# Kernel tuning notes

Measured on AMD Instinct MI355X. Metric: run time of the kernel, lower is better.

The kernel has to match this reference:

```python
import jax, jax.numpy as jnp
import numpy as np
from jax import lax

WINDOW = 8
MAX_VAL = 1.0
C1 = (0.01 * MAX_VAL) ** 2
C2 = (0.03 * MAX_VAL) ** 2


def _box_sum(x):
    # Equivalent to conv2d with an all-ones WINDOW x WINDOW kernel, groups=C, VALID padding.
    return lax.reduce_window(x, 0.0, lax.add,
                             window_dimensions=(1, 1, WINDOW, WINDOW),
                             window_strides=(1, 1, 1, 1),
                             padding='VALID')


def setup_inputs() -> dict:
    key = jax.random.key(0)
    k1, k2 = jax.random.split(key)
    shape = (32, 3, 512, 512)  # NCHW, C=3 per groups=3 conv
    groundtruth = jax.random.uniform(k1, shape, dtype=jnp.float32)
    noisy_img = jax.random.uniform(k2, shape, dtype=jnp.float32)
    return {"groundtruth": groundtruth, "noisy_img": noisy_img}


def reference(groundtruth, noisy_img):
    mu1 = _box_sum(groundtruth)
    mu2 = _box_sum(noisy_img)
    mu1_sq = mu1 * mu1
    mu2_sq = mu2 * mu2
    mu1_mu2 = mu1 * mu2
    sigma1_sq = _box_sum(groundtruth * groundtruth) - mu1_sq
    sigma2_sq = _box_sum(noisy_img * noisy_img) - mu2_sq
    sigma12 = _box_sum(groundtruth * noisy_img) - mu1_mu2
    ssim_map = ((2.0 * mu1_mu2 + C1) * (2.0 * sigma12 + C2)) / (
        (mu1_sq + mu2_sq + C1) * (sigma1_sq + sigma2_sq + C2))
    return jnp.mean(1.0 - ssim_map)
```

## Files before the change

### kernel.cpp

```cpp
#include <hip/hip_runtime.h>


#define W 512
#define H 512
#define OW 505
#define OH 505
#define TH 16
#define NSTRIP ((OH + TH - 1) / TH)
#define NIMG 96
#define NPIX (96.0 * 505.0 * 505.0)

__device__ __forceinline__ float4 ld4(const float* p) { return *(const float4*)p; }
__device__ __forceinline__ float4 f4add(float4 a, float4 b) {
    return make_float4(a.x + b.x, a.y + b.y, a.z + b.z, a.w + b.w);
}
__device__ __forceinline__ float4 f4sub(float4 a, float4 b) {
    return make_float4(a.x - b.x, a.y - b.y, a.z - b.z, a.w - b.w);
}
__device__ __forceinline__ float4 f4mul(float4 a, float4 b) {
    return make_float4(a.x * b.x, a.y * b.y, a.z * b.z, a.w * b.w);
}

__global__ void zero_ws(double* p) { *p = 0.0; }

__global__ void finalize(const double* p, float* out) {
    out[0] = 1.0f - (float)(*p / NPIX);
}

__global__ void __launch_bounds__(128, 4)
ssim_main(const float* __restrict__ gt, const float* __restrict__ ni,
          double* __restrict__ acc_out)
{
    const int t   = threadIdx.x;
    const int c0  = t * 4;
    const int img = blockIdx.y;
    const int R0  = blockIdx.x * TH;
    const int R1  = min(R0 + TH, OH);

    const float C1 = 1e-4f;
    const float C2 = 9e-4f;

    const float* gx = gt + (size_t)img * (W * H) + c0;
    const float* gy = ni + (size_t)img * (W * H) + c0;

    __shared__ float vbuf[4][520];
    __shared__ float wpart[2];

    float4 ring_x[8], ring_y[8];
    float4 vsx = make_float4(0, 0, 0, 0);
    float4 vsy = make_float4(0, 0, 0, 0);
    float4 vsq = make_float4(0, 0, 0, 0);
    float4 vsp = make_float4(0, 0, 0, 0);

#pragma unroll
    for (int k = 0; k < 7; ++k) {
        float4 x = ld4(gx + (size_t)(R0 + k) * W);
        float4 y = ld4(gy + (size_t)(R0 + k) * W);
        ring_x[k] = x; ring_y[k] = y;
        vsx = f4add(vsx, x);
        vsy = f4add(vsy, y);
        vsq = f4add(vsq, f4add(f4mul(x, x), f4mul(y, y)));
        vsp = f4add(vsp, f4mul(x, y));
    }
    ring_x[7] = make_float4(0, 0, 0, 0);
    ring_y[7] = make_float4(0, 0, 0, 0);

    float4 px = ld4(gx + (size_t)(R0 + 7) * W);
    float4 py = ld4(gy + (size_t)(R0 + 7) * W);

    float acc = 0.0f;

#define HORIZ(q, v) {                                                     \
        float4 n1 = *(float4*)&vbuf[q][c0 + 4];                           \
        float4 n2 = *(float4*)&vbuf[q][c0 + 8];                           \
        float s = ((v.x + v.y) + (v.z + v.w)) +                           \
                  ((n1.x + n1.y) + (n1.z + n1.w));                        \
        B[q][0] = s;                                                      \
        s += n2.x - v.x; B[q][1] = s;                                     \
        s += n2.y - v.y; B[q][2] = s;                                     \
        s += n2.z - v.z; B[q][3] = s;                                     \
    }

#define ROWBODY(k, slot) {                                                \
        const int r = rbase + (k);                                        \
        if (r < R1) {                                  \
            float4 cx = px, cy = py;                                      \
            if (r + 1 < R1) {    \
                px = ld4(gx + (size_t)(r + 8) * W);                       \
                py = ld4(gy + (size_t)(r + 8) * W);                       \
            }                                                             \
            float4 ox = ring_x[slot], oy = ring_y[slot];                  \
            vsx = f4add(f4sub(vsx, ox), cx);                              \
            vsy = f4add(f4sub(vsy, oy), cy);                              \
            vsq = f4add(vsq, f4sub(f4add(f4mul(cx, cx), f4mul(cy, cy)),   \
                                   f4add(f4mul(ox, ox), f4mul(oy, oy)))); \
            vsp = f4add(vsp, f4sub(f4mul(cx, cy), f4mul(ox, oy)));        \
            ring_x[slot] = cx; ring_y[slot] = cy;                         \
            *(float4*)&vbuf[0][c0] = vsx;                                 \
            *(float4*)&vbuf[1][c0] = vsy;                                 \
            *(float4*)&vbuf[2][c0] = vsq;                                 \
            *(float4*)&vbuf[3][c0] = vsp;                                 \
            __syncthreads();                                              \
            float B[4][4];                                                \
            HORIZ(0, vsx); HORIZ(1, vsy); HORIZ(2, vsq); HORIZ(3, vsp);   \
            __syncthreads();  \
            _Pragma("unroll")                                             \
            for (int j = 0; j < 4; ++j) {                                 \
                float Sx = B[0][j], Sy = B[1][j];                         \
                float Sq = B[2][j], Sp = B[3][j];                         \
                float mu12 = Sx * Sy;                                     \
                float n1v = 2.0f * mu12 + C1;                             \
                float n2v = 2.0f * (Sp - mu12) + C2;                      \
                float sx2 = Sx * Sx, sy2 = Sy * Sy;                       \
                float d1  = sx2 + sy2 + C1;                               \
                float d2  = (Sq - sx2 - sy2) + C2;                        \
                float sv  = (n1v * n2v) * __builtin_amdgcn_rcpf(d1 * d2); \
                if (c0 + j < OW) acc += sv;                               \
            }                                                             \
        }                                                                 \
    }

    for (int rbase = R0; rbase < R1; rbase += 8) {
        ROWBODY(0, 7)
        ROWBODY(1, 0)
        ROWBODY(2, 1)
        ROWBODY(3, 2)
        ROWBODY(4, 3)
        ROWBODY(5, 4)
        ROWBODY(6, 5)
        ROWBODY(7, 6)
    }

#pragma unroll
    for (int off = 32; off > 0; off >>= 1) acc += __shfl_down(acc, off);
    const int wave = t >> 6, lane = t & 63;
    if (lane == 0) wpart[wave] = acc;
    __syncthreads();
    if (t == 0) atomicAdd(acc_out, (double)(wpart[0] + wpart[1]));
}

extern "C" void kernel_launch(void* const* d_in, const int* in_sizes, int n_in,
                              void* d_out, int out_size, void* d_ws, size_t ws_size,
                              hipStream_t stream) {
    const float* gt = (const float*)d_in[0];
    const float* ni = (const float*)d_in[1];
    double* acc = (double*)d_ws;

    zero_ws<<<1, 1, 0, stream>>>(acc);
    dim3 grid(NSTRIP, NIMG);
    ssim_main<<<grid, 128, 0, stream>>>(gt, ni, acc);
    finalize<<<1, 1, 0, stream>>>(acc, (float*)d_out);
}
```

Before: 251.1 us.

## Use one wave per strip with 8 columns per lane and wave-level sync

Each block becomes a single 64-lane wavefront that handles 8 columns per lane, so the two block-wide __syncthreads per row become a wave barrier. Row prefetch is now two rows deep to hide global load latency, and the zeroing kernel is replaced by hipMemsetAsync. In exchange each lane holds twice the ring-buffer registers, which may lower occupancy, and there are half as many threads in flight per block.

```diff
diff --git a/kernel.cpp b/kernel.cpp
--- a/kernel.cpp
+++ b/kernel.cpp
@@ -21,101 +21,134 @@
     return make_float4(a.x * b.x, a.y * b.y, a.z * b.z, a.w * b.w);
 }
 
-__global__ void zero_ws(double* p) { *p = 0.0; }
-
 __global__ void finalize(const double* p, float* out) {
     out[0] = 1.0f - (float)(*p / NPIX);
 }
 
-__global__ void __launch_bounds__(128, 4)
+__global__ void __launch_bounds__(64, 2)
 ssim_main(const float* __restrict__ gt, const float* __restrict__ ni,
           double* __restrict__ acc_out)
 {
-    const int t   = threadIdx.x;
-    const int c0  = t * 4;
-    const int img = blockIdx.y;
-    const int R0  = blockIdx.x * TH;
-    const int R1  = min(R0 + TH, OH);
+    const int lane = threadIdx.x;
+    const int img  = blockIdx.y;
+    const int R0   = blockIdx.x * TH;
+    const int R1   = min(R0 + TH, OH);
+    const int c0   = lane * 8;
 
-    const float C1 = 1e-4f;
-    const float C2 = 9e-4f;
+    const float C1 = 1e-4f, C2 = 9e-4f;
 
     const float* gx = gt + (size_t)img * (W * H) + c0;
     const float* gy = ni + (size_t)img * (W * H) + c0;
 
     __shared__ float vbuf[4][520];
-    __shared__ float wpart[2];
 
-    float4 ring_x[8], ring_y[8];
-    float4 vsx = make_float4(0, 0, 0, 0);
-    float4 vsy = make_float4(0, 0, 0, 0);
-    float4 vsq = make_float4(0, 0, 0, 0);
-    float4 vsp = make_float4(0, 0, 0, 0);
+    float4 rx[8][2], ry[8][2];
+
+    float4 vsx0 = make_float4(0,0,0,0), vsx1 = make_float4(0,0,0,0);
+    float4 vsy0 = make_float4(0,0,0,0), vsy1 = make_float4(0,0,0,0);
+    float4 vsq0 = make_float4(0,0,0,0), vsq1 = make_float4(0,0,0,0);
+    float4 vsp0 = make_float4(0,0,0,0), vsp1 = make_float4(0,0,0,0);
 
 #pragma unroll
     for (int k = 0; k < 7; ++k) {
-        float4 x = ld4(gx + (size_t)(R0 + k) * W);
-        float4 y = ld4(gy + (size_t)(R0 + k) * W);
-        ring_x[k] = x; ring_y[k] = y;
-        vsx = f4add(vsx, x);
-        vsy = f4add(vsy, y);
-        vsq = f4add(vsq, f4add(f4mul(x, x), f4mul(y, y)));
-        vsp = f4add(vsp, f4mul(x, y));
+        const float* bx = gx + (size_t)(R0 + k) * W;
+        const float* by = gy + (size_t)(R0 + k) * W;
+        float4 x0 = ld4(bx), x1 = ld4(bx + 4);
+        float4 y0 = ld4(by), y1 = ld4(by + 4);
+        rx[k][0] = x0; rx[k][1] = x1; ry[k][0] = y0; ry[k][1] = y1;
+        vsx0 = f4add(vsx0, x0); vsx1 = f4add(vsx1, x1);
+        vsy0 = f4add(vsy0, y0); vsy1 = f4add(vsy1, y1);
+        vsq0 = f4add(vsq0, f4add(f4mul(x0,x0), f4mul(y0,y0)));
+        vsq1 = f4add(vsq1, f4add(f4mul(x1,x1), f4mul(y1,y1)));
+        vsp0 = f4add(vsp0, f4mul(x0,y0));
+        vsp1 = f4add(vsp1, f4mul(x1,y1));
     }
-    ring_x[7] = make_float4(0, 0, 0, 0);
-    ring_y[7] = make_float4(0, 0, 0, 0);
+    rx[7][0] = rx[7][1] = ry[7][0] = ry[7][1] = make_float4(0,0,0,0);
 
-    float4 px = ld4(gx + (size_t)(R0 + 7) * W);
-    float4 py = ld4(gy + (size_t)(R0 + 7) * W);
+    float4 pfx[2][2], pfy[2][2];
+    {
+        const float* bx = gx + (size_t)(R0 + 7) * W;
+        const float* by = gy + (size_t)(R0 + 7) * W;
+        pfx[0][0] = ld4(bx); pfx[0][1] = ld4(bx + 4);
+        pfy[0][0] = ld4(by); pfy[0][1] = ld4(by + 4);
+    }
+    {
+        const float* bx = gx + (size_t)(R0 + 8) * W;
+        const float* by = gy + (size_t)(R0 + 8) * W;
+        pfx[1][0] = ld4(bx); pfx[1][1] = ld4(bx + 4);
+        pfy[1][0] = ld4(by); pfy[1][1] = ld4(by + 4);
+    }
 
     float acc = 0.0f;
 
-#define HORIZ(q, v) {                                                     \
-        float4 n1 = *(float4*)&vbuf[q][c0 + 4];                           \
-        float4 n2 = *(float4*)&vbuf[q][c0 + 8];                           \
-        float s = ((v.x + v.y) + (v.z + v.w)) +                           \
-                  ((n1.x + n1.y) + (n1.z + n1.w));                        \
-        B[q][0] = s;                                                      \
-        s += n2.x - v.x; B[q][1] = s;                                     \
-        s += n2.y - v.y; B[q][2] = s;                                     \
-        s += n2.z - v.z; B[q][3] = s;                                     \
+#define HORIZ(S, v, n) {                                                  \
+        float T = ((v[0]+v[1])+(v[2]+v[3])) + ((v[4]+v[5])+(v[6]+v[7]));  \
+        S[0] = T;                                                         \
+        _Pragma("unroll") for (int j = 1; j < 8; ++j)                     \
+            S[j] = S[j-1] - v[j-1] + n[j-1];                              \
     }
 
 #define ROWBODY(k, slot) {                                                \
         const int r = rbase + (k);                                        \
-        if (r < R1) {                                  \
-            float4 cx = px, cy = py;                                      \
-            if (r + 1 < R1) {    \
-                px = ld4(gx + (size_t)(r + 8) * W);                       \
-                py = ld4(gy + (size_t)(r + 8) * W);                       \
+        if (r < R1) {                                   \
+            const int p = (k) & 1;                                        \
+            float4 cx0 = pfx[p][0], cx1 = pfx[p][1];                      \
+            float4 cy0 = pfy[p][0], cy1 = pfy[p][1];                      \
+            if (r + 2 < R1) {    \
+                const float* bx = gx + (size_t)(r + 9) * W;               \
+                const float* by = gy + (size_t)(r + 9) * W;               \
+                pfx[p][0] = ld4(bx); pfx[p][1] = ld4(bx + 4);             \
+                pfy[p][0] = ld4(by); pfy[p][1] = ld4(by + 4);             \
             }                                                             \
-            float4 ox = ring_x[slot], oy = ring_y[slot];                  \
-            vsx = f4add(f4sub(vsx, ox), cx);                              \
-            vsy = f4add(f4sub(vsy, oy), cy);                              \
-            vsq = f4add(vsq, f4sub(f4add(f4mul(cx, cx), f4mul(cy, cy)),   \
-                                   f4add(f4mul(ox, ox), f4mul(oy, oy)))); \
-            vsp = f4add(vsp, f4sub(f4mul(cx, cy), f4mul(ox, oy)));        \
-            ring_x[slot] = cx; ring_y[slot] = cy;                         \
-            *(float4*)&vbuf[0][c0] = vsx;                                 \
-            *(float4*)&vbuf[1][c0] = vsy;                                 \
-            *(float4*)&vbuf[2][c0] = vsq;                                 \
-            *(float4*)&vbuf[3][c0] = vsp;                                 \
-            __syncthreads();                                              \
-            float B[4][4];                                                \
-            HORIZ(0, vsx); HORIZ(1, vsy); HORIZ(2, vsq); HORIZ(3, vsp);   \
-            __syncthreads();  \
+            float4 ox0 = rx[slot][0], ox1 = rx[slot][1];                  \
+            float4 oy0 = ry[slot][0], oy1 = ry[slot][1];                  \
+            vsx0 = f4add(f4sub(vsx0, ox0), cx0);                          \
+            vsx1 = f4add(f4sub(vsx1, ox1), cx1);                          \
+            vsy0 = f4add(f4sub(vsy0, oy0), cy0);                          \
+            vsy1 = f4add(f4sub(vsy1, oy1), cy1);                          \
+            vsq0 = f4add(vsq0, f4sub(f4add(f4mul(cx0,cx0), f4mul(cy0,cy0)), \
+                                     f4add(f4mul(ox0,ox0), f4mul(oy0,oy0)))); \
+            vsq1 = f4add(vsq1, f4sub(f4add(f4mul(cx1,cx1), f4mul(cy1,cy1)), \
+                                     f4add(f4mul(ox1,ox1), f4mul(oy1,oy1)))); \
+            vsp0 = f4add(vsp0, f4sub(f4mul(cx0,cy0), f4mul(ox0,oy0)));    \
+            vsp1 = f4add(vsp1, f4sub(f4mul(cx1,cy1), f4mul(ox1,oy1)));    \
+            rx[slot][0] = cx0; rx[slot][1] = cx1;                         \
+            ry[slot][0] = cy0; ry[slot][1] = cy1;                         \
+                                  \
+            *(float4*)&vbuf[0][c0] = vsx0; *(float4*)&vbuf[0][c0+4] = vsx1; \
+            *(float4*)&vbuf[1][c0] = vsy0; *(float4*)&vbuf[1][c0+4] = vsy1; \
+            *(float4*)&vbuf[2][c0] = vsq0; *(float4*)&vbuf[2][c0+4] = vsq1; \
+            *(float4*)&vbuf[3][c0] = vsp0; *(float4*)&vbuf[3][c0+4] = vsp1; \
+            __builtin_amdgcn_sched_barrier(0);                            \
+            __builtin_amdgcn_wave_barrier();                              \
+            __builtin_amdgcn_sched_barrier(0);                            \
+                       \
+            float4 nx0 = *(float4*)&vbuf[0][c0+8], nx1 = *(float4*)&vbuf[0][c0+12]; \
+            float4 ny0 = *(float4*)&vbuf[1][c0+8], ny1 = *(float4*)&vbuf[1][c0+12]; \
+            float4 nq0 = *(float4*)&vbuf[2][c0+8], nq1 = *(float4*)&vbuf[2][c0+12]; \
+            float4 np0 = *(float4*)&vbuf[3][c0+8], np1 = *(float4*)&vbuf[3][c0+12]; \
+            float vx[8] = {vsx0.x,vsx0.y,vsx0.z,vsx0.w,vsx1.x,vsx1.y,vsx1.z,vsx1.w}; \
+            float vy[8] = {vsy0.x,vsy0.y,vsy0.z,vsy0.w,vsy1.x,vsy1.y,vsy1.z,vsy1.w}; \
+            float vq[8] = {vsq0.x,vsq0.y,vsq0.z,vsq0.w,vsq1.x,vsq1.y,vsq1.z,vsq1.w}; \
+            float vp[8] = {vsp0.x,vsp0.y,vsp0.z,vsp0.w,vsp1.x,vsp1.y,vsp1.z,vsp1.w}; \
+            float nx[8] = {nx0.x,nx0.y,nx0.z,nx0.w,nx1.x,nx1.y,nx1.z,nx1.w}; \
+            float ny[8] = {ny0.x,ny0.y,ny0.z,ny0.w,ny1.x,ny1.y,ny1.z,ny1.w}; \
+            float nq[8] = {nq0.x,nq0.y,nq0.z,nq0.w,nq1.x,nq1.y,nq1.z,nq1.w}; \
+            float np[8] = {np0.x,np0.y,np0.z,np0.w,np1.x,np1.y,np1.z,np1.w}; \
+            float Sx[8], Sy[8], Sq[8], Sp[8];                             \
+            HORIZ(Sx, vx, nx) HORIZ(Sy, vy, ny)                           \
+            HORIZ(Sq, vq, nq) HORIZ(Sp, vp, np)                           \
             _Pragma("unroll")                                             \
-            for (int j = 0; j < 4; ++j) {                                 \
-                float Sx = B[0][j], Sy = B[1][j];                         \
-                float Sq = B[2][j], Sp = B[3][j];                         \
-                float mu12 = Sx * Sy;                                     \
+            for (int j = 0; j < 8; ++j) {                                 \
+                float sx = Sx[j], sy = Sy[j];                             \
+                float mu12 = sx * sy;                                     \
                 float n1v = 2.0f * mu12 + C1;                             \
-                float n2v = 2.0f * (Sp - mu12) + C2;                      \
-                float sx2 = Sx * Sx, sy2 = Sy * Sy;                       \
+                float n2v = 2.0f * (Sp[j] - mu12) + C2;                   \
+                float sx2 = sx * sx, sy2 = sy * sy;                       \
                 float d1  = sx2 + sy2 + C1;                               \
-                float d2  = (Sq - sx2 - sy2) + C2;                        \
+                float d2  = (Sq[j] - sx2 - sy2) + C2;                     \
                 float sv  = (n1v * n2v) * __builtin_amdgcn_rcpf(d1 * d2); \
-                if (c0 + j < OW) acc += sv;                               \
+                if (c0 + j < OW) acc += sv;     \
             }                                                             \
         }                                                                 \
     }
@@ -132,11 +165,8 @@
     }
 
 #pragma unroll
-    for (int off = 32; off > 0; off >>= 1) acc += __shfl_down(acc, off);
-    const int wave = t >> 6, lane = t & 63;
-    if (lane == 0) wpart[wave] = acc;
-    __syncthreads();
-    if (t == 0) atomicAdd(acc_out, (double)(wpart[0] + wpart[1]));
+    for (int off = 32; off; off >>= 1) acc += __shfl_down(acc, off);
+    if (lane == 0) atomicAdd(acc_out, (double)acc);
 }
 
 extern "C" void kernel_launch(void* const* d_in, const int* in_sizes, int n_in,
@@ -146,8 +176,8 @@
     const float* ni = (const float*)d_in[1];
     double* acc = (double*)d_ws;
 
-    zero_ws<<<1, 1, 0, stream>>>(acc);
+    hipMemsetAsync(acc, 0, sizeof(double), stream);
     dim3 grid(NSTRIP, NIMG);
-    ssim_main<<<grid, 128, 0, stream>>>(gt, ni, acc);
+    ssim_main<<<grid, 64, 0, stream>>>(gt, ni, acc);
     finalize<<<1, 1, 0, stream>>>(acc, (float*)d_out);
 }
```

Measured after the change: 256.4 us. 1.02x slower.
